# Optimization experiments

Hardware: AMD Instinct MI355X
Metric: run time of the kernel (lower is better)

Reference implementation:

```python
import jax, jax.numpy as jnp
import numpy as np

N = 20000          # graph_size
IN_DIM = 256
H, D = 3, 64       # num_heads (hardcoded 3 in source), out_dim
E = 640000         # N * avg_degree(32)
NEG_SLOPE = 0.2    # DGL GATConv default negative_slope


def setup_inputs() -> dict:
    key = jax.random.key(0)
    ks = jax.random.split(key, 8)
    feat = jax.random.normal(ks[0], (N, IN_DIM), dtype=jnp.float32)
    W = jax.random.normal(ks[1], (IN_DIM, H * D), dtype=jnp.float32) * 0.05
    attn_l = jax.random.normal(ks[2], (H, D), dtype=jnp.float32) * 0.05
    attn_r = jax.random.normal(ks[3], (H, D), dtype=jnp.float32) * 0.05
    gat_bias = jnp.zeros((H * D,), dtype=jnp.float32)
    fc_w = jax.random.normal(ks[4], (N * H * D, 2), dtype=jnp.float32) * 0.001
    fc_b = jnp.zeros((2,), dtype=jnp.float32)
    src = jax.random.randint(ks[5], (E,), 0, N, dtype=jnp.int64)
    dst = jax.random.randint(ks[6], (E,), 0, N, dtype=jnp.int64)
    return {"feat": feat, "W": W, "attn_l": attn_l, "attn_r": attn_r,
            "gat_bias": gat_bias, "fc_w": fc_w, "fc_b": fc_b,
            "src": src, "dst": dst}


def reference(feat, W, attn_l, attn_r, gat_bias, fc_w, fc_b, src, dst):
    n = feat.shape[0]
    # GATConv: projected multi-head features [N, H, D]
    h = (feat @ W).reshape(n, H, D)
    el = jnp.einsum('nhd,hd->nh', h, attn_l)   # [N, H]
    er = jnp.einsum('nhd,hd->nh', h, attn_r)   # [N, H]
    # per-edge raw attention logits, LeakyReLU(el[src] + er[dst])
    e = jax.nn.leaky_relu(el[src] + er[dst], negative_slope=NEG_SLOPE)  # [E, H]
    # edge-softmax grouped by destination node (stable)
    m = jax.ops.segment_max(e, dst, num_segments=n)   # [N, H]
    ex = jnp.exp(e - m[dst])
    denom = jax.ops.segment_sum(ex, dst, num_segments=n)  # [N, H]
    alpha = ex / denom[dst]                            # [E, H]
    # weighted message aggregation: out[v] = sum_{(u->v)} alpha * h[u]
    msg = h[src] * alpha[:, :, None]                   # [E, H, D]
    out = jax.ops.segment_sum(msg, dst, num_segments=n)  # [N, H, D]
    out = out + gat_bias.reshape(H, D)                 # GATConv bias
    out = jax.nn.relu(out)                             # self.activation
    # Flatten(start_dim=0) -> Linear(N*H*D, 2)
    return out.reshape(-1) @ fc_w + fc_b               # [2]
```

## Files before the change

### kernel.cpp

```cpp
#include <hip/hip_runtime.h>
#include <hip/hip_bf16.h>
#include <cstdint>
#include <cstddef>

#define INDIM  256
#define HD     192
#define NHEADS 3
#define NEG_SLOPE 0.2f
#define ELLPAD 96
#define BSHIFT 7
#define NBUCK  160
#define BCAP   4608
#define P1CHUNK 2048

typedef __attribute__((ext_vector_type(8))) short short8;
typedef __attribute__((ext_vector_type(4))) float f32x4;

__device__ __forceinline__ float wave_sum(float v) {
#pragma unroll
    for (int o = 32; o; o >>= 1) v += __shfl_xor(v, o, 64);
    return v;
}

__global__ __launch_bounds__(256) void prep_kernel(
    const float* __restrict__ W, __hip_bfloat16* __restrict__ Wt,
    int* __restrict__ gCur)
{
    const int b = blockIdx.x, tid = threadIdx.x;
    if (b == 0) {
        if (tid < NBUCK) gCur[tid] = 0;
        return;
    }
    int n = b - 1;
    Wt[n * 256 + tid] = __float2bfloat16(W[tid * HD + n]);
}

__global__ __launch_bounds__(256) void gemm_bucket_kernel(
    const float* __restrict__ feat,
    const __hip_bfloat16* __restrict__ Wt,
    const float* __restrict__ attn_l, const float* __restrict__ attn_r,
    __hip_bfloat16* __restrict__ hb, float* __restrict__ el,
    float* __restrict__ er, int M,
    const int* __restrict__ src, const int* __restrict__ dst,
    int* __restrict__ gCur, int2* __restrict__ pairs,
    int E, int gemmBlocks)
{
    const int tid = threadIdx.x;
    if (blockIdx.x >= gemmBlocks) {
        __shared__ int cnt[NBUCK];
        __shared__ int base[NBUCK];
        const int e0 = (blockIdx.x - gemmBlocks) * P1CHUNK;
        if (tid < NBUCK) cnt[tid] = 0;
        __syncthreads();
        int d[8], s[8], b[8], l[8];
#pragma unroll
        for (int u = 0; u < 8; u++) {
            int e = e0 + u * 256 + tid;
            if (e < E) {
                d[u] = dst[e]; s[u] = src[e];
                b[u] = d[u] >> BSHIFT;
                l[u] = atomicAdd(&cnt[b[u]], 1);
            } else b[u] = -1;
        }
        __syncthreads();
        if (tid < NBUCK && cnt[tid] > 0) base[tid] = atomicAdd(&gCur[tid], cnt[tid]);
        __syncthreads();
#pragma unroll
        for (int u = 0; u < 8; u++) {
            if (b[u] >= 0) {
                int idx = base[b[u]] + l[u];
                if (idx < BCAP)
                    pairs[(size_t)b[u] * BCAP + idx] = make_int2(d[u], s[u]);
            }
        }
        return;
    }
    __shared__ __hip_bfloat16 As[64][40];
    __shared__ __hip_bfloat16 Bs[192][40];
    const int lane = tid & 63, w = tid >> 6;
    const int q = lane >> 4, ll = lane & 15;
    const int row0 = blockIdx.x * 64;

    f32x4 acc[12];
#pragma unroll
    for (int c = 0; c < 12; c++) acc[c] = (f32x4){0.f, 0.f, 0.f, 0.f};

    const int sr = tid >> 2, sk = (tid & 3) * 8;

    for (int k0 = 0; k0 < INDIM; k0 += 32) {
        __syncthreads();
        float4 a0 = make_float4(0.f, 0.f, 0.f, 0.f), a1 = a0;
        int grow = row0 + sr;
        if (grow < M) {
            const float* ap = feat + (size_t)grow * INDIM + k0 + sk;
            a0 = *(const float4*)ap;
            a1 = *(const float4*)(ap + 4);
        }
        __hip_bfloat16 ab[8] = {__float2bfloat16(a0.x), __float2bfloat16(a0.y),
                                __float2bfloat16(a0.z), __float2bfloat16(a0.w),
                                __float2bfloat16(a1.x), __float2bfloat16(a1.y),
                                __float2bfloat16(a1.z), __float2bfloat16(a1.w)};
        *(uint4*)&As[sr][sk] = *(const uint4*)ab;
        if (tid < HD) {
            const __hip_bfloat16* bp = Wt + (size_t)tid * INDIM + k0;
            uint4 b0 = *(const uint4*)bp;
            uint4 b1 = *(const uint4*)(bp + 8);
            uint4 b2 = *(const uint4*)(bp + 16);
            uint4 b3 = *(const uint4*)(bp + 24);
            *(uint4*)&Bs[tid][0]  = b0;
            *(uint4*)&Bs[tid][8]  = b1;
            *(uint4*)&Bs[tid][16] = b2;
            *(uint4*)&Bs[tid][24] = b3;
        }
        __syncthreads();

        short8 af = *(const short8*)&As[w * 16 + ll][q * 8];
#pragma unroll
        for (int c = 0; c < 12; c++) {
            short8 bf = *(const short8*)&Bs[c * 16 + ll][q * 8];
            acc[c] = __builtin_amdgcn_mfma_f32_16x16x32_bf16(af, bf, acc[c], 0, 0, 0);
        }
    }

    float al[12], ar[12];
#pragma unroll
    for (int c = 0; c < 12; c++) {
        al[c] = attn_l[c * 16 + ll];
        ar[c] = attn_r[c * 16 + ll];
    }
    float sl[3][4], sr_[3][4];
#pragma unroll
    for (int hd = 0; hd < 3; hd++)
#pragma unroll
        for (int i = 0; i < 4; i++) {
            float a = 0.f, b = 0.f;
#pragma unroll
            for (int f = 0; f < 4; f++) {
                a = fmaf(acc[hd * 4 + f][i], al[hd * 4 + f], a);
                b = fmaf(acc[hd * 4 + f][i], ar[hd * 4 + f], b);
            }
            sl[hd][i] = a; sr_[hd][i] = b;
        }
#pragma unroll
    for (int hd = 0; hd < 3; hd++)
#pragma unroll
        for (int i = 0; i < 4; i++)
#pragma unroll
            for (int off = 1; off < 16; off <<= 1) {
                sl[hd][i]  += __shfl_xor(sl[hd][i],  off, 64);
                sr_[hd][i] += __shfl_xor(sr_[hd][i], off, 64);
            }
#pragma unroll
    for (int c = 0; c < 12; c++)
#pragma unroll
        for (int i = 0; i < 4; i++) {
            int row = row0 + w * 16 + q * 4 + i;
            if (row < M)
                hb[(size_t)row * HD + c * 16 + ll] = __float2bfloat16(acc[c][i]);
        }
    if (ll == 0) {
#pragma unroll
        for (int i = 0; i < 4; i++) {
            int row = row0 + w * 16 + q * 4 + i;
            if (row < M) {
#pragma unroll
                for (int hd = 0; hd < 3; hd++) {
                    el[row * 3 + hd] = sl[hd][i];
                    er[row * 3 + hd] = sr_[hd][i];
                }
            }
        }
    }
}

__global__ __launch_bounds__(256) void ell_build_kernel(
    const int2* __restrict__ pairs, const int* __restrict__ gCur,
    int* __restrict__ ell, int* __restrict__ deg, int N)
{
    __shared__ int cur[128];
    const int b = blockIdx.x;
    const int tid = threadIdx.x;
    if (tid < 128) cur[tid] = 0;
    __syncthreads();
    const int cnt = min(gCur[b], BCAP);
    const int2* pp = pairs + (size_t)b * BCAP;
    for (int i = tid; i < cnt; i += 256) {
        int2 p = pp[i];
        int r = atomicAdd(&cur[p.x & 127], 1);
        if (r < ELLPAD) ell[(size_t)p.x * ELLPAD + r] = p.y;
    }
    __syncthreads();
    int node = (b << BSHIFT) + tid;
    if (tid < 128 && node < N) deg[node] = min(cur[tid], ELLPAD);
}

__global__ __launch_bounds__(256) void gat_node_kernel(
    const __hip_bfloat16* __restrict__ h, const float* __restrict__ el,
    const float* __restrict__ er, const int* __restrict__ deg,
    const int* __restrict__ ell, const float* __restrict__ gbias,
    const float* __restrict__ fc_w, float* __restrict__ pA,
    float* __restrict__ pB, int N)
{
    __shared__ float4 sE[4][64];

    const int tid = threadIdx.x;
    const int lane = tid & 63, wslot = tid >> 6;
    const int v = blockIdx.x * 4 + wslot;
    if (v >= N) return;

    const int cnt = deg[v];
    const int* rowp = ell + (size_t)v * ELLPAD;
    const float er0 = er[v * 3 + 0], er1 = er[v * 3 + 1], er2 = er[v * 3 + 2];

    float acc0 = 0.f, acc1 = 0.f, acc2 = 0.f;
    float d0 = 0.f, d1 = 0.f, d2 = 0.f;
    const __hip_bfloat16* hl = h + lane;

    for (int chunk = 0; chunk < cnt; chunk += 64) {
        const int i = chunk + lane;
        float w0 = 0.f, w1 = 0.f, w2 = 0.f;
        int s = 0;
        if (i < cnt) {
            s = rowp[i];
            const float* ep = el + s * 3;
            float l0 = ep[0] + er0;
            float l1 = ep[1] + er1;
            float l2 = ep[2] + er2;
            l0 = l0 > 0.f ? l0 : NEG_SLOPE * l0;
            l1 = l1 > 0.f ? l1 : NEG_SLOPE * l1;
            l2 = l2 > 0.f ? l2 : NEG_SLOPE * l2;
            w0 = __expf(l0); w1 = __expf(l1); w2 = __expf(l2);
        }
        d0 += w0; d1 += w1; d2 += w2;
        sE[wslot][lane] = make_float4(__int_as_float(s), w0, w1, w2);
        __asm__ volatile("s_waitcnt lgkmcnt(0)" ::: "memory");

        const int rem = min(cnt - chunk, 64);
        const int nR = (rem + 7) & ~7;
        for (int j = 0; j < nR; j += 8) {
            float4 e[8];
#pragma unroll
            for (int u = 0; u < 8; u++) e[u] = sE[wslot][j + u];
            float x0[8], x1[8], x2[8];
#pragma unroll
            for (int u = 0; u < 8; u++) {
                const __hip_bfloat16* p = hl + (size_t)__float_as_int(e[u].x) * HD;
                x0[u] = __bfloat162float(p[0]);
                x1[u] = __bfloat162float(p[64]);
                x2[u] = __bfloat162float(p[128]);
            }
#pragma unroll
            for (int u = 0; u < 8; u++) {
                acc0 = fmaf(e[u].y, x0[u], acc0);
                acc1 = fmaf(e[u].z, x1[u], acc1);
                acc2 = fmaf(e[u].w, x2[u], acc2);
            }
        }
    }

    d0 = wave_sum(d0); d1 = wave_sum(d1); d2 = wave_sum(d2);

    float o0 = (d0 > 0.f) ? acc0 / d0 : 0.f;
    float o1 = (d1 > 0.f) ? acc1 / d1 : 0.f;
    float o2 = (d2 > 0.f) ? acc2 / d2 : 0.f;
    o0 = fmaxf(o0 + gbias[lane], 0.f);
    o1 = fmaxf(o1 + gbias[64 + lane], 0.f);
    o2 = fmaxf(o2 + gbias[128 + lane], 0.f);

    const size_t bidx = (size_t)v * HD;
    float2 w0v = ((const float2*)fc_w)[bidx + lane];
    float2 w1v = ((const float2*)fc_w)[bidx + 64 + lane];
    float2 w2v = ((const float2*)fc_w)[bidx + 128 + lane];
    float f0 = fmaf(o0, w0v.x, fmaf(o1, w1v.x, o2 * w2v.x));
    float f1 = fmaf(o0, w0v.y, fmaf(o1, w1v.y, o2 * w2v.y));

    f0 = wave_sum(f0); f1 = wave_sum(f1);
    if (lane == 0) { pA[v] = f0; pB[v] = f1; }
}

__global__ __launch_bounds__(1024) void final_reduce(const float* __restrict__ pA,
                                                     const float* __restrict__ pB,
                                                     const float* __restrict__ fc_b,
                                                     float* __restrict__ out, int nb)
{
    int tid = threadIdx.x;
    float s0 = 0.f, s1 = 0.f;
    for (int i = tid; i < nb; i += 1024) { s0 += pA[i]; s1 += pB[i]; }
    s0 = wave_sum(s0); s1 = wave_sum(s1);
    __shared__ float sh[32];
    int lane = tid & 63, w = tid >> 6;
    if (lane == 0) { sh[w * 2] = s0; sh[w * 2 + 1] = s1; }
    __syncthreads();
    if (tid == 0) {
        float t0 = 0.f, t1 = 0.f;
#pragma unroll
        for (int i = 0; i < 16; i++) { t0 += sh[i * 2]; t1 += sh[i * 2 + 1]; }
        out[0] = t0 + fc_b[0];
        out[1] = t1 + fc_b[1];
    }
}

extern "C" void kernel_launch(void* const* d_in, const int* in_sizes, int n_in,
                              void* d_out, int out_size, void* d_ws, size_t ws_size,
                              hipStream_t stream)
{
    const float* feat   = (const float*)d_in[0];
    const float* W      = (const float*)d_in[1];
    const float* attn_l = (const float*)d_in[2];
    const float* attn_r = (const float*)d_in[3];
    const float* gbias  = (const float*)d_in[4];
    const float* fc_w   = (const float*)d_in[5];
    const float* fc_b   = (const float*)d_in[6];
    const int*   src    = (const int*)d_in[7];
    const int*   dst    = (const int*)d_in[8];

    const int N = in_sizes[0] / INDIM;
    const int E = in_sizes[7];
    const int nBuck = (N + 127) >> BSHIFT;

    __hip_bfloat16* Wt = (__hip_bfloat16*)d_ws;
    __hip_bfloat16* hb = Wt + HD * INDIM;
    float* el = (float*)(hb + (size_t)N * HD);
    float* er = el + (size_t)N * 3;
    int* gCur = (int*)(er + (size_t)N * 3);
    int* deg  = gCur + NBUCK;
    int* ell  = deg + N;
    int2* pairs = (int2*)(ell + (size_t)N * ELLPAD);
    float* pA = (float*)(pairs + (size_t)NBUCK * BCAP);
    float* pB = pA + N;

    prep_kernel<<<1 + HD, 256, 0, stream>>>(W, Wt, gCur);

    const int gemmBlocks = (N + 63) / 64;
    const int p1Blocks = (E + P1CHUNK - 1) / P1CHUNK;
    gemm_bucket_kernel<<<gemmBlocks + p1Blocks, 256, 0, stream>>>(
        feat, Wt, attn_l, attn_r, hb, el, er, N,
        src, dst, gCur, pairs, E, gemmBlocks);

    ell_build_kernel<<<nBuck, 256, 0, stream>>>(pairs, gCur, ell, deg, N);

    gat_node_kernel<<<(N + 3) / 4, 256, 0, stream>>>(hb, el, er, deg, ell,
                                                     gbias, fc_w, pA, pB, N);
    final_reduce<<<1, 1024, 0, stream>>>(pA, pB, fc_b, (float*)d_out, N);
}
```

Before: 162.1 us.

## Build ELL adjacency directly with global atomics, drop bucket pass and pad el/er

Replaces the two-pass bucketed edge sort (shared-memory bucket counts, a pairs buffer and a separate ell_build kernel) with direct global atomicAdd on per-node degree counters that place each source straight into the ELL row. This removes one kernel launch and the intermediate pairs round-trip through memory. The attention logit arrays el/er are padded to stride 4 so the node kernel can read them as single float4 loads. In exchange it issues 640K global atomics scattered over 20K counters, and the zeroing of deg moves into the prep kernel.

```diff
diff --git a/kernel.cpp b/kernel.cpp
--- a/kernel.cpp
+++ b/kernel.cpp
@@ -8,9 +8,6 @@
 #define NHEADS 3
 #define NEG_SLOPE 0.2f
 #define ELLPAD 96
-#define BSHIFT 7
-#define NBUCK  160
-#define BCAP   4608
 #define P1CHUNK 2048
 
 typedef __attribute__((ext_vector_type(8))) short short8;
@@ -24,14 +21,15 @@
 
 __global__ __launch_bounds__(256) void prep_kernel(
     const float* __restrict__ W, __hip_bfloat16* __restrict__ Wt,
-    int* __restrict__ gCur)
+    int* __restrict__ deg, int N, int zblk)
 {
     const int b = blockIdx.x, tid = threadIdx.x;
-    if (b == 0) {
-        if (tid < NBUCK) gCur[tid] = 0;
+    if (b < zblk) {
+        int i = b * 256 + tid;
+        if (i < N) deg[i] = 0;
         return;
     }
-    int n = b - 1;
+    int n = b - zblk;
     Wt[n * 256 + tid] = __float2bfloat16(W[tid * HD + n]);
 }
 
@@ -42,37 +40,26 @@
     __hip_bfloat16* __restrict__ hb, float* __restrict__ el,
     float* __restrict__ er, int M,
     const int* __restrict__ src, const int* __restrict__ dst,
-    int* __restrict__ gCur, int2* __restrict__ pairs,
+    int* __restrict__ deg, int* __restrict__ ell,
     int E, int gemmBlocks)
 {
     const int tid = threadIdx.x;
     if (blockIdx.x >= gemmBlocks) {
-        __shared__ int cnt[NBUCK];
-        __shared__ int base[NBUCK];
         const int e0 = (blockIdx.x - gemmBlocks) * P1CHUNK;
-        if (tid < NBUCK) cnt[tid] = 0;
-        __syncthreads();
-        int d[8], s[8], b[8], l[8];
+        int d[8], s[8], r[8];
 #pragma unroll
         for (int u = 0; u < 8; u++) {
             int e = e0 + u * 256 + tid;
-            if (e < E) {
-                d[u] = dst[e]; s[u] = src[e];
-                b[u] = d[u] >> BSHIFT;
-                l[u] = atomicAdd(&cnt[b[u]], 1);
-            } else b[u] = -1;
-        }
-        __syncthreads();
-        if (tid < NBUCK && cnt[tid] > 0) base[tid] = atomicAdd(&gCur[tid], cnt[tid]);
-        __syncthreads();
-#pragma unroll
-        for (int u = 0; u < 8; u++) {
-            if (b[u] >= 0) {
-                int idx = base[b[u]] + l[u];
-                if (idx < BCAP)
-                    pairs[(size_t)b[u] * BCAP + idx] = make_int2(d[u], s[u]);
-            }
-        }
+            if (e < E) { d[u] = dst[e]; s[u] = src[e]; }
+            else d[u] = -1;
+        }
+#pragma unroll
+        for (int u = 0; u < 8; u++)
+            if (d[u] >= 0) r[u] = atomicAdd(&deg[d[u]], 1);
+#pragma unroll
+        for (int u = 0; u < 8; u++)
+            if (d[u] >= 0 && r[u] < ELLPAD)
+                ell[(size_t)d[u] * ELLPAD + r[u]] = s[u];
         return;
     }
     __shared__ __hip_bfloat16 As[64][40];
@@ -165,33 +152,12 @@
             if (row < M) {
 #pragma unroll
                 for (int hd = 0; hd < 3; hd++) {
-                    el[row * 3 + hd] = sl[hd][i];
-                    er[row * 3 + hd] = sr_[hd][i];
+                    el[row * 4 + hd] = sl[hd][i];
+                    er[row * 4 + hd] = sr_[hd][i];
                 }
             }
         }
     }
-}
-
-__global__ __launch_bounds__(256) void ell_build_kernel(
-    const int2* __restrict__ pairs, const int* __restrict__ gCur,
-    int* __restrict__ ell, int* __restrict__ deg, int N)
-{
-    __shared__ int cur[128];
-    const int b = blockIdx.x;
-    const int tid = threadIdx.x;
-    if (tid < 128) cur[tid] = 0;
-    __syncthreads();
-    const int cnt = min(gCur[b], BCAP);
-    const int2* pp = pairs + (size_t)b * BCAP;
-    for (int i = tid; i < cnt; i += 256) {
-        int2 p = pp[i];
-        int r = atomicAdd(&cur[p.x & 127], 1);
-        if (r < ELLPAD) ell[(size_t)p.x * ELLPAD + r] = p.y;
-    }
-    __syncthreads();
-    int node = (b << BSHIFT) + tid;
-    if (tid < 128 && node < N) deg[node] = min(cur[tid], ELLPAD);
 }
 
 __global__ __launch_bounds__(256) void gat_node_kernel(
@@ -208,9 +174,10 @@
     const int v = blockIdx.x * 4 + wslot;
     if (v >= N) return;
 
-    const int cnt = deg[v];
+    const int cnt = min(deg[v], ELLPAD);
     const int* rowp = ell + (size_t)v * ELLPAD;
-    const float er0 = er[v * 3 + 0], er1 = er[v * 3 + 1], er2 = er[v * 3 + 2];
+    const float4 erv = ((const float4*)er)[v];
+    const float er0 = erv.x, er1 = erv.y, er2 = erv.z;
 
     float acc0 = 0.f, acc1 = 0.f, acc2 = 0.f;
     float d0 = 0.f, d1 = 0.f, d2 = 0.f;
@@ -222,10 +189,10 @@
         int s = 0;
         if (i < cnt) {
             s = rowp[i];
-            const float* ep = el + s * 3;
-            float l0 = ep[0] + er0;
-            float l1 = ep[1] + er1;
-            float l2 = ep[2] + er2;
+            const float4 le = ((const float4*)el)[s];
+            float l0 = le.x + er0;
+            float l1 = le.y + er1;
+            float l2 = le.z + er2;
             l0 = l0 > 0.f ? l0 : NEG_SLOPE * l0;
             l1 = l1 > 0.f ? l1 : NEG_SLOPE * l1;
             l2 = l2 > 0.f ? l2 : NEG_SLOPE * l2;
@@ -316,28 +283,24 @@
 
     const int N = in_sizes[0] / INDIM;
     const int E = in_sizes[7];
-    const int nBuck = (N + 127) >> BSHIFT;
 
     __hip_bfloat16* Wt = (__hip_bfloat16*)d_ws;
     __hip_bfloat16* hb = Wt + HD * INDIM;
     float* el = (float*)(hb + (size_t)N * HD);
-    float* er = el + (size_t)N * 3;
-    int* gCur = (int*)(er + (size_t)N * 3);
-    int* deg  = gCur + NBUCK;
+    float* er = el + (size_t)N * 4;
+    int* deg  = (int*)(er + (size_t)N * 4);
     int* ell  = deg + N;
-    int2* pairs = (int2*)(ell + (size_t)N * ELLPAD);
-    float* pA = (float*)(pairs + (size_t)NBUCK * BCAP);
+    float* pA = (float*)(ell + (size_t)N * ELLPAD);
     float* pB = pA + N;
 
-    prep_kernel<<<1 + HD, 256, 0, stream>>>(W, Wt, gCur);
+    const int zblk = (N + 255) >> 8;
+    prep_kernel<<<zblk + HD, 256, 0, stream>>>(W, Wt, deg, N, zblk);
 
     const int gemmBlocks = (N + 63) / 64;
     const int p1Blocks = (E + P1CHUNK - 1) / P1CHUNK;
     gemm_bucket_kernel<<<gemmBlocks + p1Blocks, 256, 0, stream>>>(
         feat, Wt, attn_l, attn_r, hb, el, er, N,
-        src, dst, gCur, pairs, E, gemmBlocks);
-
-    ell_build_kernel<<<nBuck, 256, 0, stream>>>(pairs, gCur, ell, deg, N);
+        src, dst, deg, ell, E, gemmBlocks);
 
     gat_node_kernel<<<(N + 3) / 4, 256, 0, stream>>>(hb, el, er, deg, ell,
                                                      gbias, fc_w, pA, pB, N);
```

New measurement: 175.1 us. +8.0%, slower.
